# Performance work log

Measured on AMD Instinct MI355X. Metric: run time of the kernel, lower is better.

## Reference

```python
import jax, jax.numpy as jnp
import numpy as np

B, S, H, NH = 4, 2048, 1024, 16
D = H // NH  # head width = 64
SCALE = 1.0 / np.sqrt(np.float32(H))  # NOTE: module scales by rsqrt(hidden_size), not head_width
EPS = 1e-5


def setup_inputs() -> dict:
    key = jax.random.key(0)
    ks = jax.random.split(key, 12)
    def lin(k):
        kw, kb = jax.random.split(k)
        return (jax.random.normal(kw, (H, H), jnp.float32) * 0.02,
                jax.random.normal(kb, (H,), jnp.float32) * 0.02)
    Wq, bq = lin(ks[0]); Wk, bk = lin(ks[1]); Wv, bv = lin(ks[2]); Wm, bm = lin(ks[3])
    q = jax.random.normal(ks[4], (B, S, H), jnp.float32)
    k = jax.random.normal(ks[5], (B, S, H), jnp.float32)
    v = jax.random.normal(ks[6], (B, S, H), jnp.float32)
    # causal mask: True positions are masked with -inf (matches masked_fill semantics)
    mask = jnp.broadcast_to(jnp.triu(jnp.ones((S, S), bool), k=1), (B, S, S))
    gamma = jnp.ones((H,), jnp.float32)
    beta = jnp.zeros((H,), jnp.float32)
    return {"q": q, "k": k, "v": v, "mask": mask,
            "Wq": Wq, "bq": bq, "Wk": Wk, "bk": bk, "Wv": Wv, "bv": bv,
            "Wm": Wm, "bm": bm, "gamma": gamma, "beta": beta}


def layer_norm(x, gamma, beta):
    mu = jnp.mean(x, axis=-1, keepdims=True)
    var = jnp.mean(jnp.square(x - mu), axis=-1, keepdims=True)
    return (x - mu) * jax.lax.rsqrt(var + EPS) * gamma + beta


def reference(q, k, v, mask, Wq, bq, Wk, bk, Wv, bv, Wm, bm, gamma, beta):
    residual = q
    # projections, split into heads: [B, NH, S, D]
    qh = (q @ Wq.T + bq).reshape(B, S, NH, D).transpose(0, 2, 1, 3)
    kh = (k @ Wk.T + bk).reshape(B, S, NH, D).transpose(0, 2, 1, 3)
    vh = (v @ Wv.T + bv).reshape(B, S, NH, D).transpose(0, 2, 1, 3)
    scores = jnp.einsum('bhsd,bhtd->bhst', qh, kh) * SCALE
    scores = jnp.where(mask[:, None, :, :], -jnp.inf, scores)
    attn = jax.nn.softmax(scores, axis=-1)  # dropout is identity (p=0 / eval)
    ctx = jnp.einsum('bhst,bhtd->bhsd', attn, vh)
    ctx = ctx.transpose(0, 2, 1, 3).reshape(B, S, H)
    out = ctx @ Wm.T + bm
    out = layer_norm(out + residual, gamma, beta)
    return out, attn
```

## Files before the change

### kernel.cpp

```cpp
#include <hip/hip_runtime.h>
#include <hip/hip_bf16.h>

#define S_LEN   2048
#define NHEAD   16
#define HID     1024
#define HDIM    64
#define ATT_SCALE 0.03125f
#define LN_EPS  1e-5f
#define EXP_C1  0.04508422002778011f
#define EXP_C2  (-11.541560327111707f)

using bf16x8 = __attribute__((ext_vector_type(8))) short;
using f32x4  = __attribute__((ext_vector_type(4))) float;
using u16x8  = __attribute__((ext_vector_type(8))) unsigned short;
typedef unsigned short u16;

__device__ __forceinline__ u16 f2b(float f) {
  union { float f; unsigned u; } v; v.f = f;
  unsigned r = v.u + 0x7fffu + ((v.u >> 16) & 1u);
  return (u16)(r >> 16);
}

__device__ __forceinline__ float fexp2(float x) {
  return __builtin_amdgcn_exp2f(x);
}

__device__ __forceinline__ unsigned cvtpk(float a, float b) {
  unsigned r;
  asm("v_cvt_pk_bf16_f32 %0, %1, %2" : "=v"(r) : "v"(a), "v"(b));
  return r;
}

__device__ __forceinline__ f32x4 mfma16(bf16x8 a, bf16x8 b, f32x4 c) {
  return __builtin_amdgcn_mfma_f32_16x16x32_bf16(a, b, c, 0, 0, 0);
}

__device__ __forceinline__ void gld_lds16(const u16* g, void* l) {
  __builtin_amdgcn_global_load_lds(
      (const __attribute__((address_space(1))) void*)g,
      (__attribute__((address_space(3))) void*)l, 16, 0, 0);
}

__global__ void cvt_f32_bf16(const float* __restrict__ src, u16* __restrict__ dst, int n4) {
  int i = blockIdx.x * blockDim.x + threadIdx.x;
  int stride = gridDim.x * blockDim.x;
  for (; i < n4; i += stride) {
    float4 v = ((const float4*)src)[i];
    ushort4 o;
    o.x = f2b(v.x); o.y = f2b(v.y); o.z = f2b(v.z); o.w = f2b(v.w);
    ((ushort4*)dst)[i] = o;
  }
}

template<int EPI>
__global__ __launch_bounds__(256) void gemm_bt(
    const u16* __restrict__ A, const u16* __restrict__ W,
    const float* __restrict__ bias, u16* __restrict__ out_b,
    float* __restrict__ out_f, int M, int N, int K)
{
  __shared__ __align__(16) u16 As[128 * 64];
  __shared__ __align__(16) u16 Bs[128 * 64];
  const int t = threadIdx.x;
  const int m0 = blockIdx.y * 128, n0 = blockIdx.x * 128;
  const int w = t >> 6, lane = t & 63, g = lane >> 4, c = lane & 15;
  const int wr = w >> 1, wc = w & 1;

  f32x4 acc[4][4] = {};

  for (int k0 = 0; k0 < K; k0 += 64) {
    __syncthreads();
#pragma unroll
    for (int it = 0; it < 4; ++it) {
      int chunk = it * 256 + t;
      int row = chunk >> 3, cf = (chunk & 7) * 8;
      gld_lds16(&A[(long)(m0 + row) * K + k0 + cf], &As[(it * 256 + (t & ~63)) * 8]);
      gld_lds16(&W[(long)(n0 + row) * K + k0 + cf], &Bs[(it * 256 + (t & ~63)) * 8]);
    }
    __syncthreads();
#pragma unroll
    for (int kk = 0; kk < 2; ++kk) {
      bf16x8 am[4], bn[4];
#pragma unroll
      for (int m = 0; m < 4; ++m)
        am[m] = *(const bf16x8*)(&As[(wr * 64 + m * 16 + c) * 64 + kk * 32 + g * 8]);
#pragma unroll
      for (int n = 0; n < 4; ++n)
        bn[n] = *(const bf16x8*)(&Bs[(wc * 64 + n * 16 + c) * 64 + kk * 32 + g * 8]);
#pragma unroll
      for (int m = 0; m < 4; ++m)
#pragma unroll
        for (int n = 0; n < 4; ++n)
          acc[m][n] = mfma16(am[m], bn[n], acc[m][n]);
    }
  }

#pragma unroll
  for (int m = 0; m < 4; ++m)
#pragma unroll
    for (int n = 0; n < 4; ++n)
#pragma unroll
      for (int r = 0; r < 4; ++r) {
        int grow = m0 + wr * 64 + m * 16 + g * 4 + r;
        int gcol = n0 + wc * 64 + n * 16 + c;
        float v = acc[m][n][r];
        if (EPI == 0) {
          v += bias[gcol];
          int b = grow >> 11, s = grow & 2047;
          int h = gcol >> 6, d = gcol & 63;
          out_b[(((long)(b * 16 + h) * 2048 + s) << 6) + d] = f2b(v);
        } else {
          out_f[(long)grow * N + gcol] = v;
        }
      }
}

__global__ __launch_bounds__(256) void transpose_v(const u16* __restrict__ vh,
                                                   u16* __restrict__ vt) {
  __shared__ __align__(16) u16 tile[64 * 72];
  const int t = threadIdx.x;
  const u16* src = vh + ((long)blockIdx.y * 2048 + blockIdx.x * 64) * 64;
#pragma unroll
  for (int it = 0; it < 2; ++it) {
    int chunk = it * 256 + t;
    int s = chunk >> 3, d0 = (chunk & 7) * 8;
    *(int4*)(&tile[s * 72 + d0]) = *(const int4*)(&src[s * 64 + d0]);
  }
  __syncthreads();
  u16* dst = vt + (long)blockIdx.y * 64 * 2048 + blockIdx.x * 64;
#pragma unroll
  for (int it = 0; it < 2; ++it) {
    int chunk = it * 256 + t;
    int d = chunk >> 3, s0 = (chunk & 7) * 8;
    u16x8 v;
#pragma unroll
    for (int x = 0; x < 8; ++x) v[x] = tile[(s0 + x) * 72 + d];
    *(u16x8*)(&dst[(long)d * 2048 + s0]) = v;
  }
}

__global__ __launch_bounds__(512, 4) void attn_kernel(
    const u16* __restrict__ qh, const u16* __restrict__ kh,
    const u16* __restrict__ vt, u16* __restrict__ ctx,
    float* __restrict__ attn)
{
  __shared__ __align__(16) char lds[81920];
  const int t = threadIdx.x, w = t >> 6, lane = t & 63, g = lane >> 4, c = lane & 15;
  const int n = blockIdx.x;
  const int bh = (n & 7) * 8 + ((n >> 3) & 7);
  const int qtb = 15 - (n >> 6);
  const int q0 = qtb * 128;
  const int ktmax = qtb * 2 + 1;
  const long kvbase = (long)bh * 2048 * 64;

  bf16x8 qa[2];
  {
    const u16* qp = qh + kvbase + (long)(q0 + w * 16 + c) * 64 + g * 8;
    qa[0] = *(const bf16x8*)(qp);
    qa[1] = *(const bf16x8*)(qp + 32);
  }
  const int qpos = q0 + w * 16 + c;

  const int srow = t >> 3, sc8 = t & 7;
  const int ksoff = srow * 64 + ((sc8 ^ (srow & 7)) * 8);
  const u16* kbase = kh + kvbase;
  const u16* vbase = vt + (long)(bh * 64 + srow) * 2048 + ((sc8 ^ (srow & 7)) * 8);

  float lsum = 0.f;
  {
    gld_lds16(kbase + ksoff, lds + w * 1024);
    gld_lds16(kbase + 4096 + ksoff, lds + 8192 + w * 1024);
    for (int p = 0; p <= qtb; ++p) {
      const int kb = (p & 1) * 16384;
      if (p < qtb) {
        const int nb = ((p + 1) & 1) * 16384;
        gld_lds16(kbase + (long)(p + 1) * 8192 + ksoff, lds + nb + w * 1024);
        gld_lds16(kbase + (long)(p + 1) * 8192 + 4096 + ksoff, lds + nb + 8192 + w * 1024);
        asm volatile("s_waitcnt vmcnt(2)" ::: "memory");
      } else {
        asm volatile("s_waitcnt vmcnt(0)" ::: "memory");
      }
      __builtin_amdgcn_sched_barrier(0);
      __builtin_amdgcn_s_barrier();
      __builtin_amdgcn_sched_barrier(0);
      f32x4 sacc[8] = {};
      __builtin_amdgcn_s_setprio(1);
#pragma unroll
      for (int sub = 0; sub < 8; ++sub) {
        int row = sub * 16 + c;
#pragma unroll
        for (int kk = 0; kk < 2; ++kk) {
          bf16x8 av = *(const bf16x8*)(lds + kb + row * 128 + (((kk * 4 + g) ^ (c & 7)) << 4));
          sacc[sub] = mfma16(av, qa[kk], sacc[sub]);
        }
      }
      __builtin_amdgcn_s_setprio(0);
#pragma unroll
      for (int sub = 0; sub < 8; ++sub)
#pragma unroll
        for (int r = 0; r < 4; ++r) {
          int kpos = p * 128 + sub * 16 + g * 4 + r;
          float e = fexp2(fmaf(sacc[sub][r], EXP_C1, EXP_C2));
          lsum += (kpos > qpos) ? 0.f : e;
        }
      __builtin_amdgcn_sched_barrier(0);
      __builtin_amdgcn_s_barrier();
    }
  }
  lsum += __shfl_xor(lsum, 16, 64);
  lsum += __shfl_xor(lsum, 32, 64);
  const float ri = 1.f / lsum;

  char* const Ps = lds + 32768 + w * 2048;
  char* const Pf = lds + 49152 + w * 4096;
  f32x4 oacc[4] = {};
  gld_lds16(kbase + ksoff, lds + w * 1024);
  gld_lds16(vbase, lds + 16384 + w * 1024);
  for (int kt = 0; kt <= ktmax; ++kt) {
    const int kb = (kt & 1) * 8192;
    if (kt < ktmax) {
      const int nb = ((kt + 1) & 1) * 8192;
      gld_lds16(kbase + (long)(kt + 1) * 4096 + ksoff, lds + nb + w * 1024);
      gld_lds16(vbase + (kt + 1) * 64, lds + 16384 + nb + w * 1024);
      if (kt == 0) { asm volatile("s_waitcnt vmcnt(2)" ::: "memory"); }
      else         { asm volatile("s_waitcnt vmcnt(6)" ::: "memory"); }
    } else {
      asm volatile("s_waitcnt vmcnt(4)" ::: "memory");
    }
    __builtin_amdgcn_sched_barrier(0);
    __builtin_amdgcn_s_barrier();
    __builtin_amdgcn_sched_barrier(0);
    f32x4 sacc[4] = {};
    __builtin_amdgcn_s_setprio(1);
#pragma unroll
    for (int sub = 0; sub < 4; ++sub) {
      int row = sub * 16 + c;
#pragma unroll
      for (int kk = 0; kk < 2; ++kk) {
        bf16x8 av = *(const bf16x8*)(lds + kb + row * 128 + (((kk * 4 + g) ^ (c & 7)) << 4));
        sacc[sub] = mfma16(av, qa[kk], sacc[sub]);
      }
    }
    __builtin_amdgcn_s_setprio(0);
#pragma unroll
    for (int sub = 0; sub < 4; ++sub) {
      float p[4];
#pragma unroll
      for (int r = 0; r < 4; ++r) {
        int kpos = kt * 64 + sub * 16 + g * 4 + r;
        float e = fexp2(fmaf(sacc[sub][r], EXP_C1, EXP_C2)) * ri;
        p[r] = (kpos > qpos) ? 0.f : e;
      }
      f32x4 pv4 = { p[0], p[1], p[2], p[3] };
      int kgrp = sub * 4 + g;
      *(f32x4*)(Pf + c * 256 + ((kgrp ^ c) & 15) * 16) = pv4;
      uint2 pk = { cvtpk(p[0], p[1]), cvtpk(p[2], p[3]) };
      int chunk = sub * 2 + (g >> 1);
      *(uint2*)(Ps + c * 128 + ((chunk ^ (c & 7)) << 4) + (g & 1) * 8) = pk;
    }
    {
      float* arow0 = attn + ((long)bh * 2048 + q0 + w * 16) * 2048 + kt * 64;
#pragma unroll
      for (int j = 0; j < 4; ++j) {
        int row = j * 4 + g;
        f32x4 pv = *(const f32x4*)(Pf + row * 256 + ((c ^ row) & 15) * 16);
        *(f32x4*)(arow0 + (long)row * 2048 + c * 4) = pv;
      }
    }
    __builtin_amdgcn_s_setprio(1);
#pragma unroll
    for (int kk = 0; kk < 2; ++kk) {
      bf16x8 pa = *(const bf16x8*)(Ps + c * 128 + (((kk * 4 + g) ^ (c & 7)) << 4));
#pragma unroll
      for (int db = 0; db < 4; ++db) {
        bf16x8 vb = *(const bf16x8*)(lds + 16384 + kb + (db * 16 + c) * 128 + (((kk * 4 + g) ^ (c & 7)) << 4));
        oacc[db] = mfma16(pa, vb, oacc[db]);
      }
    }
    __builtin_amdgcn_s_setprio(0);
    __builtin_amdgcn_sched_barrier(0);
    __builtin_amdgcn_s_barrier();
  }

  {
    int b = bh >> 4, h = bh & 15;
#pragma unroll
    for (int db = 0; db < 4; ++db)
#pragma unroll
      for (int r = 0; r < 4; ++r) {
        int s = q0 + w * 16 + g * 4 + r;
        ctx[(long)(b * 2048 + s) * 1024 + h * 64 + db * 16 + c] = f2b(oacc[db][r]);
      }
  }

  {
    f32x4 z = { 0.f, 0.f, 0.f, 0.f };
    for (int row = w; row < 128; row += 8) {
      float* rp = attn + ((long)bh * 2048 + q0 + row) * 2048;
      for (int col = q0 + 128 + lane * 4; col < 2048; col += 256)
        *(f32x4*)(rp + col) = z;
    }
  }
}

__global__ __launch_bounds__(256) void ln_kernel(
    const float* __restrict__ y, const float* __restrict__ bm,
    const float* __restrict__ resid, const float* __restrict__ gamma,
    const float* __restrict__ beta, float* __restrict__ out)
{
  __shared__ float red[8];
  const long row = blockIdx.x;
  const int t = threadIdx.x, w = t >> 6, lane = t & 63;
  const float4* yp = (const float4*)(y + row * 1024);
  const float4* rp = (const float4*)(resid + row * 1024);
  float4 x = yp[t], rv = rp[t], bv = ((const float4*)bm)[t];
  x.x += rv.x + bv.x; x.y += rv.y + bv.y; x.z += rv.z + bv.z; x.w += rv.w + bv.w;

  float s1 = x.x + x.y + x.z + x.w;
#pragma unroll
  for (int o = 32; o; o >>= 1) s1 += __shfl_xor(s1, o, 64);
  if (!lane) red[w] = s1;
  __syncthreads();
  float mean = (red[0] + red[1] + red[2] + red[3]) * (1.f / 1024.f);

  float dx = x.x - mean, dy = x.y - mean, dz = x.z - mean, dw = x.w - mean;
  float s2 = dx * dx + dy * dy + dz * dz + dw * dw;
#pragma unroll
  for (int o = 32; o; o >>= 1) s2 += __shfl_xor(s2, o, 64);
  if (!lane) red[4 + w] = s2;
  __syncthreads();
  float var = (red[4] + red[5] + red[6] + red[7]) * (1.f / 1024.f);
  float rs = rsqrtf(var + LN_EPS);

  float4 gv = ((const float4*)gamma)[t], be = ((const float4*)beta)[t];
  float4 o4;
  o4.x = dx * rs * gv.x + be.x;
  o4.y = dy * rs * gv.y + be.y;
  o4.z = dz * rs * gv.z + be.z;
  o4.w = dw * rs * gv.w + be.w;
  ((float4*)(out + row * 1024))[t] = o4;
}

extern "C" void kernel_launch(void* const* d_in, const int* in_sizes, int n_in,
                              void* d_out, int out_size, void* d_ws, size_t ws_size,
                              hipStream_t stream) {
  const float* q     = (const float*)d_in[0];
  const float* k     = (const float*)d_in[1];
  const float* v     = (const float*)d_in[2];
  const float* Wq    = (const float*)d_in[4];
  const float* bq    = (const float*)d_in[5];
  const float* Wk    = (const float*)d_in[6];
  const float* bk    = (const float*)d_in[7];
  const float* Wv    = (const float*)d_in[8];
  const float* bv    = (const float*)d_in[9];
  const float* Wm    = (const float*)d_in[10];
  const float* bm    = (const float*)d_in[11];
  const float* gamma = (const float*)d_in[12];
  const float* beta  = (const float*)d_in[13];

  float* out  = (float*)d_out;
  float* attn = out + 8388608;

  char* ws = (char*)d_ws;
  u16* qh   = (u16*)(ws);
  u16* kh   = (u16*)(ws + 16777216);
  u16* vt   = (u16*)(ws + 33554432);
  u16* ctx  = (u16*)(ws + 50331648);
  u16* Wqb  = (u16*)(ws + 67108864);
  u16* Wkb  = Wqb + 1048576;
  u16* Wvb  = Wkb + 1048576;
  u16* Wmb  = Wvb + 1048576;
  u16* xb   = (u16*)(ws + 75497472);
  u16* vh   = (u16*)(ws + 92274688);
  float* y  = (float*)(ws + 75497472);

  const int M = 8192, N = 1024, K = 1024;
  dim3 blk(256);
  dim3 ggrid(8, 64);

  cvt_f32_bf16<<<512, blk, 0, stream>>>(Wq, Wqb, 262144);
  cvt_f32_bf16<<<512, blk, 0, stream>>>(Wk, Wkb, 262144);
  cvt_f32_bf16<<<512, blk, 0, stream>>>(Wv, Wvb, 262144);
  cvt_f32_bf16<<<512, blk, 0, stream>>>(Wm, Wmb, 262144);

  cvt_f32_bf16<<<2048, blk, 0, stream>>>(q, xb, 2097152);
  gemm_bt<0><<<ggrid, blk, 0, stream>>>(xb, Wqb, bq, qh, nullptr, M, N, K);
  cvt_f32_bf16<<<2048, blk, 0, stream>>>(k, xb, 2097152);
  gemm_bt<0><<<ggrid, blk, 0, stream>>>(xb, Wkb, bk, kh, nullptr, M, N, K);
  cvt_f32_bf16<<<2048, blk, 0, stream>>>(v, xb, 2097152);
  gemm_bt<0><<<ggrid, blk, 0, stream>>>(xb, Wvb, bv, vh, nullptr, M, N, K);

  transpose_v<<<dim3(32, 64), blk, 0, stream>>>(vh, vt);

  attn_kernel<<<1024, 512, 0, stream>>>(qh, kh, vt, ctx, attn);

  gemm_bt<1><<<ggrid, blk, 0, stream>>>(ctx, Wmb, nullptr, nullptr, y, M, N, K);

  ln_kernel<<<8192, blk, 0, stream>>>(y, bm, q, gamma, beta, out);
}
```

Measured before the change: 512.6 us.

## Move masked-zero fill of attention matrix into extra blocks of projection GEMMs

The zero-writing of the strictly upper causal region of the fp32 attention output is taken out of the attention kernel. It is spread over 43 extra block rows appended to each of the three QKV projection GEMM launches, with each launch covering one third of the tiles. The goal is to hide this large store-only traffic behind compute-bound GEMM blocks and shorten the attention kernel's tail. The cost is extra grid blocks competing for memory bandwidth with the GEMMs, and correctness relies on attn_kernel never writing those tiles.

```diff
diff --git a/kernel.cpp b/kernel.cpp
--- a/kernel.cpp
+++ b/kernel.cpp
@@ -56,11 +56,31 @@
 __global__ __launch_bounds__(256) void gemm_bt(
     const u16* __restrict__ A, const u16* __restrict__ W,
     const float* __restrict__ bias, u16* __restrict__ out_b,
-    float* __restrict__ out_f, int M, int N, int K)
+    float* __restrict__ out_f, int M, int N, int K,
+    float* __restrict__ fill, int fphase)
 {
   __shared__ __align__(16) u16 As[128 * 64];
   __shared__ __align__(16) u16 Bs[128 * 64];
   const int t = threadIdx.x;
+
+  if (blockIdx.y >= 64) {
+    int unit = ((blockIdx.y - 64) * 8 + blockIdx.x) * 3 + fphase;
+    if (unit < 1024) {
+      int bh = unit >> 4, qtb = unit & 15;
+      int w4 = (15 - qtb) * 32;
+      if (w4 > 0) {
+        f32x4* base = (f32x4*)(fill + ((long)bh * 2048 + qtb * 128) * 2048
+                                    + (qtb + 1) * 128);
+        f32x4 z = { 0.f, 0.f, 0.f, 0.f };
+        for (int r = 0; r < 128; ++r) {
+          f32x4* rp = base + (long)r * 512;
+          for (int cc = t; cc < w4; cc += 256) rp[cc] = z;
+        }
+      }
+    }
+    return;
+  }
+
   const int m0 = blockIdx.y * 128, n0 = blockIdx.x * 128;
   const int w = t >> 6, lane = t & 63, g = lane >> 4, c = lane & 15;
   const int wr = w >> 1, wc = w & 1;
@@ -290,15 +310,6 @@
         int s = q0 + w * 16 + g * 4 + r;
         ctx[(long)(b * 2048 + s) * 1024 + h * 64 + db * 16 + c] = f2b(oacc[db][r]);
       }
-  }
-
-  {
-    f32x4 z = { 0.f, 0.f, 0.f, 0.f };
-    for (int row = w; row < 128; row += 8) {
-      float* rp = attn + ((long)bh * 2048 + q0 + row) * 2048;
-      for (int col = q0 + 128 + lane * 4; col < 2048; col += 256)
-        *(f32x4*)(rp + col) = z;
-    }
   }
 }
 
@@ -376,6 +387,7 @@
   const int M = 8192, N = 1024, K = 1024;
   dim3 blk(256);
   dim3 ggrid(8, 64);
+  dim3 ggridF(8, 64 + 43);
 
   cvt_f32_bf16<<<512, blk, 0, stream>>>(Wq, Wqb, 262144);
   cvt_f32_bf16<<<512, blk, 0, stream>>>(Wk, Wkb, 262144);
@@ -383,17 +395,17 @@
   cvt_f32_bf16<<<512, blk, 0, stream>>>(Wm, Wmb, 262144);
 
   cvt_f32_bf16<<<2048, blk, 0, stream>>>(q, xb, 2097152);
-  gemm_bt<0><<<ggrid, blk, 0, stream>>>(xb, Wqb, bq, qh, nullptr, M, N, K);
+  gemm_bt<0><<<ggridF, blk, 0, stream>>>(xb, Wqb, bq, qh, nullptr, M, N, K, attn, 0);
   cvt_f32_bf16<<<2048, blk, 0, stream>>>(k, xb, 2097152);
-  gemm_bt<0><<<ggrid, blk, 0, stream>>>(xb, Wkb, bk, kh, nullptr, M, N, K);
+  gemm_bt<0><<<ggridF, blk, 0, stream>>>(xb, Wkb, bk, kh, nullptr, M, N, K, attn, 1);
   cvt_f32_bf16<<<2048, blk, 0, stream>>>(v, xb, 2097152);
-  gemm_bt<0><<<ggrid, blk, 0, stream>>>(xb, Wvb, bv, vh, nullptr, M, N, K);
+  gemm_bt<0><<<ggridF, blk, 0, stream>>>(xb, Wvb, bv, vh, nullptr, M, N, K, attn, 2);
 
   transpose_v<<<dim3(32, 64), blk, 0, stream>>>(vh, vt);
 
   attn_kernel<<<1024, 512, 0, stream>>>(qh, kh, vt, ctx, attn);
 
-  gemm_bt<1><<<ggrid, blk, 0, stream>>>(ctx, Wmb, nullptr, nullptr, y, M, N, K);
+  gemm_bt<1><<<ggrid, blk, 0, stream>>>(ctx, Wmb, nullptr, nullptr, y, M, N, K, nullptr, 0);
 
   ln_kernel<<<8192, blk, 0, stream>>>(y, bm, q, gamma, beta, out);
 }
```

After: 522.7 us. About the same (+2.0%).
